# Kernel optimization log

Hardware: AMD Instinct MI355X
Metric: run time of the kernel (lower is better)

The kernel has to match this reference:

```python
import jax, jax.numpy as jnp
import numpy as np

N, E, DIM, HEADS, EDGE_DIM = 50000, 800000, 128, 4, 1
C = DIM // HEADS  # per-head channels
EPS = 1e-5


def graph_ln(h, w, b):
    # PyG LayerNorm, mode='graph', batch=None: normalize over ALL nodes+features
    mu = h.mean()
    hc = h - mu
    std = jnp.sqrt(jnp.mean(hc * hc))
    return hc / (std + EPS) * w + b


def setup_inputs() -> dict:
    key = jax.random.key(0)
    ks = jax.random.split(key, 16)
    s = 1.0 / np.sqrt(DIM)
    return {
        "x": jax.random.normal(ks[0], (N, DIM), jnp.float32),
        "edge_index": jax.random.randint(ks[1], (2, E), 0, N, jnp.int32),
        "edge_weight": jax.random.uniform(ks[2], (E,), jnp.float32),
        "edge_attr": jax.random.normal(ks[3], (E, EDGE_DIM), jnp.float32),
        # GCNConv params
        "W_gcn": jax.random.normal(ks[4], (DIM, DIM), jnp.float32) * s,
        "b_gcn": jnp.zeros((DIM,), jnp.float32),
        # GATv2Conv params (share_weights=True -> single lin)
        "W_l": jax.random.normal(ks[5], (DIM, DIM), jnp.float32) * s,
        "b_l": jnp.zeros((DIM,), jnp.float32),
        "W_edge": jax.random.normal(ks[6], (EDGE_DIM, DIM), jnp.float32),
        "att": jax.random.normal(ks[7], (HEADS, C), jnp.float32) * (1.0 / np.sqrt(C)),
        "b_gat": jnp.zeros((DIM,), jnp.float32),
        # norms
        "gcn_nw": jnp.ones((DIM,), jnp.float32), "gcn_nb": jnp.zeros((DIM,), jnp.float32),
        "gat_nw": jnp.ones((DIM,), jnp.float32), "gat_nb": jnp.zeros((DIM,), jnp.float32),
        "out_nw": jnp.ones((DIM,), jnp.float32), "out_nb": jnp.zeros((DIM,), jnp.float32),
        "alpha": jnp.ones((2,), jnp.float32),
    }


def reference(x, edge_index, edge_weight, edge_attr, W_gcn, b_gcn, W_l, b_l,
              W_edge, att, b_gat, gcn_nw, gcn_nb, gat_nw, gat_nb, out_nw, out_nb, alpha):
    src, dst = edge_index[0], edge_index[1]

    # ---- GCN branch (normalize=True, add_self_loops=False) ----
    deg = jax.ops.segment_sum(edge_weight, dst, num_segments=N)
    dis = jnp.where(deg > 0, jax.lax.rsqrt(jnp.maximum(deg, 1e-30)), 0.0)
    norm = dis[src] * edge_weight * dis[dst]  # [E]
    xw = x @ W_gcn  # [N, DIM]
    h = jax.ops.segment_sum(norm[:, None] * xw[src], dst, num_segments=N) + b_gcn
    gcn_out = x + jax.nn.gelu(graph_ln(h, gcn_nw, gcn_nb), approximate=False)

    # ---- GATv2 branch (share_weights=True, edge_dim=1) ----
    xl = (x @ W_l + b_l).reshape(N, HEADS, C)
    e = (edge_attr @ W_edge).reshape(E, HEADS, C)
    z = jax.nn.leaky_relu(xl[dst] + xl[src] + e, negative_slope=0.2)  # [E,H,C]
    logits = jnp.einsum('ehc,hc->eh', z, att)  # [E,H]
    m = jax.ops.segment_max(logits, dst, num_segments=N)  # [N,H]
    a = jnp.exp(logits - m[dst])
    denom = jax.ops.segment_sum(a, dst, num_segments=N)
    a = a / (denom[dst] + 1e-16)  # softmax over incoming edges per dst, per head
    msg = xl[src] * a[:, :, None]  # [E,H,C]
    g = jax.ops.segment_sum(msg, dst, num_segments=N).reshape(N, DIM) + b_gat
    gat_out = x + jax.nn.gelu(graph_ln(g, gat_nw, gat_nb), approximate=False)

    # ---- fuse ----
    w = jax.nn.softmax(alpha)
    fused = w[0] * gcn_out + w[1] * gat_out
    return jax.nn.gelu(graph_ln(fused, out_nw, out_nb), approximate=False)
```

## Files before the change

### kernel.cpp

```cpp
#include <hip/hip_runtime.h>
#include <math.h>

#define DIM 128
#define HEADS 4
#define EPS 1e-5f
#define NBLK 1024

__device__ __forceinline__ float us2f(unsigned short u) {
  union { unsigned int i; float f; } c; c.i = ((unsigned int)u) << 16; return c.f;
}
__device__ __forceinline__ unsigned short f2us(float f) {
  union { float ff; unsigned int i; } c; c.ff = f;
  return (unsigned short)((c.i + 0x7FFFu + ((c.i >> 16) & 1u)) >> 16);
}
__device__ __forceinline__ float ldf(const void* p, size_t i, int fl32) {
  return fl32 ? ((const float*)p)[i] : us2f(((const unsigned short*)p)[i]);
}
__device__ __forceinline__ float gelu_exact(float v) {
  return 0.5f * v * (1.0f + erff(v * 0.7071067811865475f));
}

__device__ __forceinline__ int packed_pos(int c) { return ((c & ~1) << 1) | (c & 1); }

__global__ void __launch_bounds__(256)
k_detect(const unsigned short* __restrict__ x, long n, int* __restrict__ dflag) {
  long lim = n < 8192 ? n : 8192;
  int bad = 0;
  for (long i = threadIdx.x; i < lim; i += 256) {
    float v = us2f(x[i]);
    float a = fabsf(v);
    if (!(a == 0.0f || (a > 1e-30f && a < 1e3f))) bad++;
  }
  __shared__ int sb[256];
  sb[threadIdx.x] = bad;
  __syncthreads();
  for (int off = 128; off > 0; off >>= 1) {
    if ((int)threadIdx.x < off) sb[threadIdx.x] += sb[threadIdx.x + off];
    __syncthreads();
  }
  if (threadIdx.x == 0) dflag[0] = (sb[0] > 32) ? 1 : 0;
}

__global__ void k_deg_cnt(const int* __restrict__ dst, const void* __restrict__ ew,
                          float* __restrict__ deg, int* __restrict__ cnt,
                          int* __restrict__ rank, int E, const int* __restrict__ df) {
  const int fl32 = *df;
  int e = blockIdx.x * blockDim.x + threadIdx.x;
  if (e < E) {
    int d = dst[e];
    rank[e] = atomicAdd(&cnt[d], 1);
    float w = ldf(ew, e, fl32);
    if (isfinite(w)) atomicAdd(&deg[d], w);
  }
}

__global__ void __launch_bounds__(256)
k_scan(const int* __restrict__ cnt, int* __restrict__ off, int N) {
  __shared__ int part[256];
  int t = threadIdx.x;
  int chunk = (N + 255) / 256;
  int lo = t * chunk;
  int hi = lo + chunk; if (hi > N) hi = N;
  int s = 0;
  for (int i = lo; i < hi; ++i) s += (cnt[i] + 3) & ~3;
  part[t] = s;
  __syncthreads();
  if (t == 0) {
    int run = 0;
    for (int j = 0; j < 256; ++j) { int tmp = part[j]; part[j] = run; run += tmp; }
    off[N] = run;
  }
  __syncthreads();
  int run = part[t];
  for (int i = lo; i < hi; ++i) { off[i] = run; run += (cnt[i] + 3) & ~3; }
}

__global__ void k_scatter(const int* __restrict__ src, const int* __restrict__ dst,
                          const void* __restrict__ ew, const void* __restrict__ ea,
                          const float* __restrict__ deg, const int* __restrict__ off,
                          const int* __restrict__ rank, int4* __restrict__ csr,
                          int E, const int* __restrict__ df) {
  const int fl32 = *df;
  int e = blockIdx.x * blockDim.x + threadIdx.x;
  if (e >= E) return;
  int d = dst[e], s = src[e];
  int pos = off[d] + rank[e];
  float ds = deg[s], dd = deg[d];
  float disS = (ds > 0.0f) ? rsqrtf(fmaxf(ds, 1e-30f)) : 0.0f;
  float disD = (dd > 0.0f) ? rsqrtf(fmaxf(dd, 1e-30f)) : 0.0f;
  float nm = disS * ldf(ew, e, fl32) * disD;
  if (!isfinite(nm)) nm = 0.0f;
  float eav = ldf(ea, e, fl32);
  if (!isfinite(eav)) eav = 0.0f;
  csr[pos] = make_int4(s, __float_as_int(nm), __float_as_int(eav), 1);
}

__global__ void __launch_bounds__(128)
k_gemm(const void* __restrict__ x, const void* __restrict__ Wg,
       const void* __restrict__ Wl, const void* __restrict__ bl,
       unsigned short* __restrict__ packed, int N, const int* __restrict__ df) {
  const int fl32 = *df;
  const int R = 16;
  __shared__ float xs[R][DIM];
  int c = threadIdx.x;
  int r0 = blockIdx.x * R;
  for (int r = 0; r < R; ++r) {
    int row = r0 + r;
    xs[r][c] = (row < N) ? ldf(x, (size_t)row * DIM + c, fl32) : 0.0f;
  }
  __syncthreads();
  float accg[R], accl[R];
  float blc = ldf(bl, c, fl32);
  #pragma unroll
  for (int r = 0; r < R; ++r) { accg[r] = 0.0f; accl[r] = blc; }
  for (int k = 0; k < DIM; ++k) {
    float wg = ldf(Wg, k * DIM + c, fl32);
    float wl = ldf(Wl, k * DIM + c, fl32);
    #pragma unroll
    for (int r = 0; r < R; ++r) {
      accg[r] = fmaf(xs[r][k], wg, accg[r]);
      accl[r] = fmaf(xs[r][k], wl, accl[r]);
    }
  }
  int pos = packed_pos(c);
  for (int r = 0; r < R; ++r) {
    int row = r0 + r;
    if (row < N) {
      float ag = accg[r], al = accl[r];
      if (!isfinite(ag)) ag = 0.0f;
      if (!isfinite(al)) al = 0.0f;
      packed[(size_t)row * 256 + pos] = f2us(al);
      packed[(size_t)row * 256 + pos + 2] = f2us(ag);
    }
  }
}

__global__ void __launch_bounds__(256)
k_mega(const int* __restrict__ off, const int* __restrict__ cnt,
       const int4* __restrict__ csr, const unsigned short* __restrict__ packed,
       const void* __restrict__ Wed, const void* __restrict__ att,
       const void* __restrict__ bgcn, const void* __restrict__ bgat,
       float* __restrict__ h, float* __restrict__ g,
       double* __restrict__ pA, double* __restrict__ pB, int N,
       const int* __restrict__ df) {
  const int fl32 = *df;
  int wid = threadIdx.x >> 6;
  int lane = threadIdx.x & 63;
  int node = blockIdx.x * 4 + wid;
  if (node >= N) return;
  int c0 = lane * 2;
  float wd0 = ldf(Wed, c0, fl32), wd1 = ldf(Wed, c0 + 1, fl32);
  float at0 = ldf(att, c0, fl32), at1 = ldf(att, c0 + 1, fl32);
  int beg = off[node], endP = off[node + 1];
  int realdeg = cnt[node];
  ushort4 xd = *(const ushort4*)(packed + (size_t)node * 256 + lane * 4);
  float xd0 = us2f(xd.x), xd1 = us2f(xd.y);
  float mx = -INFINITY, den = 0.f;
  float ga0 = 0.f, ga1 = 0.f, hc0 = 0.f, hc1 = 0.f;

#define GATH(ce) (*(const ushort4*)(packed + (size_t)(ce).x * 256 + lane * 4))
#define STEP(ce, v) {                                                     \
    float nm = __int_as_float((ce).y), eav = __int_as_float((ce).z);      \
    float vx = us2f((v).x), vy = us2f((v).y);                             \
    float z0 = xd0 + vx + eav * wd0; z0 = (z0 > 0.f) ? z0 : 0.2f * z0;    \
    float z1 = xd1 + vy + eav * wd1; z1 = (z1 > 0.f) ? z1 : 0.2f * z1;    \
    float dot = z0 * at0 + z1 * at1;                                      \
    dot += __shfl_xor(dot, 1);                                            \
    dot += __shfl_xor(dot, 2);                                            \
    dot += __shfl_xor(dot, 4);                                            \
    dot += __shfl_xor(dot, 8);                                            \
    if (!isfinite(dot)) dot = 0.0f;                                       \
    dot = (ce).w ? dot : -1e30f;                                          \
    float e = __expf(-fabsf(dot - mx));                                   \
    bool up = dot > mx;                                                   \
    float corr = up ? e : 1.0f;                                           \
    float w = up ? 1.0f : e;                                              \
    if (!(ce).w) w = 0.0f;                                                \
    mx = up ? dot : mx;                                                   \
    den = fmaf(den, corr, w);                                             \
    ga0 = fmaf(ga0, corr, w * vx);                                        \
    ga1 = fmaf(ga1, corr, w * vy);                                        \
    hc0 = fmaf(nm, us2f((v).z), hc0);                                     \
    hc1 = fmaf(nm, us2f((v).w), hc1);                                     \
  }

  if (beg < endP) {
    int4 ca = csr[beg], cb = csr[beg + 1], cc = csr[beg + 2], cd = csr[beg + 3];
    ushort4 va = GATH(ca), vb = GATH(cb), vc = GATH(cc), vd = GATH(cd);
    for (int i = beg; i < endP; i += 4) {
      int4 da = ca, db = cb, dc = cc, dd = cd;
      ushort4 wa = va, wb = vb, wc = vc, wdv = vd;
      if (i + 4 < endP) {
        ca = csr[i + 4]; cb = csr[i + 5]; cc = csr[i + 6]; cd = csr[i + 7];
        va = GATH(ca); vb = GATH(cb); vc = GATH(cc); vd = GATH(cd);
      }
      STEP(da, wa); STEP(db, wb); STEP(dc, wc); STEP(dd, wdv);
    }
  }
#undef STEP
#undef GATH

  float inv = (realdeg > 0) ? 1.0f / (den + 1e-16f) : 0.0f;
  ga0 *= inv; ga1 *= inv;
  if (!isfinite(ga0)) ga0 = 0.0f;
  if (!isfinite(ga1)) ga1 = 0.0f;
  if (!isfinite(hc0)) hc0 = 0.0f;
  if (!isfinite(hc1)) hc1 = 0.0f;
  *(float2*)(h + (size_t)node * DIM + c0) = make_float2(hc0, hc1);
  *(float2*)(g + (size_t)node * DIM + c0) = make_float2(ga0, ga1);
  float hA0 = hc0 + ldf(bgcn, c0, fl32), hA1 = hc1 + ldf(bgcn, c0 + 1, fl32);
  float gB0 = ga0 + ldf(bgat, c0, fl32), gB1 = ga1 + ldf(bgat, c0 + 1, fl32);
  double sA  = (double)hA0 + (double)hA1;
  double sA2 = (double)hA0 * hA0 + (double)hA1 * hA1;
  double sB  = (double)gB0 + (double)gB1;
  double sB2 = (double)gB0 * gB0 + (double)gB1 * gB1;
  #pragma unroll
  for (int o = 32; o > 0; o >>= 1) {
    sA  += __shfl_xor(sA, o);
    sA2 += __shfl_xor(sA2, o);
    sB  += __shfl_xor(sB, o);
    sB2 += __shfl_xor(sB2, o);
  }
  if (lane == 0) {
    pA[2 * node] = sA; pA[2 * node + 1] = sA2;
    pB[2 * node] = sB; pB[2 * node + 1] = sB2;
  }
}

__device__ __forceinline__ void ln_params(double S, double S2, double M, float* mu_out, float* sc_out) {
  double mu = S / M;
  double v = S2 / M - mu * mu;
  if (!(v > 0.0)) v = 0.0;
  float fmu = (float)mu;
  float sc = 1.0f / ((float)sqrt(v) + EPS);
  if (!isfinite(fmu)) fmu = 0.0f;
  if (!isfinite(sc)) sc = 0.0f;
  *mu_out = fmu; *sc_out = sc;
}

__global__ void __launch_bounds__(256)
k_fin12(const double* __restrict__ pA, const double* __restrict__ pB, int nblk,
        const void* __restrict__ alpha, float* __restrict__ params, double M,
        const int* __restrict__ df) {
  const int fl32 = *df;
  __shared__ double l1[256], l2[256], l3[256], l4[256];
  double a = 0, b = 0, c = 0, d = 0;
  for (int j = threadIdx.x; j < nblk; j += 256) {
    a += pA[2 * j]; b += pA[2 * j + 1];
    c += pB[2 * j]; d += pB[2 * j + 1];
  }
  l1[threadIdx.x] = a; l2[threadIdx.x] = b; l3[threadIdx.x] = c; l4[threadIdx.x] = d;
  __syncthreads();
  for (int off = 128; off > 0; off >>= 1) {
    if ((int)threadIdx.x < off) {
      l1[threadIdx.x] += l1[threadIdx.x + off];
      l2[threadIdx.x] += l2[threadIdx.x + off];
      l3[threadIdx.x] += l3[threadIdx.x + off];
      l4[threadIdx.x] += l4[threadIdx.x + off];
    }
    __syncthreads();
  }
  if (threadIdx.x == 0) {
    ln_params(l1[0], l2[0], M, &params[0], &params[1]);
    ln_params(l3[0], l4[0], M, &params[2], &params[3]);
    float a0 = ldf(alpha, 0, fl32), a1 = ldf(alpha, 1, fl32);
    if (!isfinite(a0)) a0 = 0.0f;
    if (!isfinite(a1)) a1 = 0.0f;
    float mx = fmaxf(a0, a1);
    float e0 = expf(a0 - mx), e1 = expf(a1 - mx);
    float inv = 1.0f / (e0 + e1);
    params[4] = e0 * inv;
    params[5] = e1 * inv;
  }
}

__global__ void __launch_bounds__(256)
k_fin3(const double* __restrict__ pC, float* __restrict__ params, double M) {
  __shared__ double l1[256], l2[256];
  double a = 0, b = 0;
  for (int j = threadIdx.x; j < NBLK; j += 256) { a += pC[2 * j]; b += pC[2 * j + 1]; }
  l1[threadIdx.x] = a; l2[threadIdx.x] = b;
  __syncthreads();
  for (int off = 128; off > 0; off >>= 1) {
    if ((int)threadIdx.x < off) {
      l1[threadIdx.x] += l1[threadIdx.x + off];
      l2[threadIdx.x] += l2[threadIdx.x + off];
    }
    __syncthreads();
  }
  if (threadIdx.x == 0) ln_params(l1[0], l2[0], M, &params[6], &params[7]);
}

__global__ void __launch_bounds__(256)
k_fuse(const void* __restrict__ x, float* h, const float* __restrict__ g,
       const void* __restrict__ b_gcn, const void* __restrict__ b_gat,
       const void* __restrict__ gcn_nw, const void* __restrict__ gcn_nb,
       const void* __restrict__ gat_nw, const void* __restrict__ gat_nb,
       const float* __restrict__ params, double* __restrict__ pC, long n,
       const int* __restrict__ df) {
  const int fl32 = *df;
  float mu1 = params[0], sc1 = params[1], mu2 = params[2], sc2 = params[3];
  float w0 = params[4], w1 = params[5];
  double s = 0.0, s2 = 0.0;
  long stride = (long)gridDim.x * blockDim.x;
  for (long i = (long)blockIdx.x * blockDim.x + threadIdx.x; i < n; i += stride) {
    size_t c = (size_t)(i & (DIM - 1));
    float xv = ldf(x, i, fl32);
    float hv = h[i] + ldf(b_gcn, c, fl32);
    float gv = g[i] + ldf(b_gat, c, fl32);
    float go = xv + gelu_exact((hv - mu1) * sc1 * ldf(gcn_nw, c, fl32) + ldf(gcn_nb, c, fl32));
    float ao = xv + gelu_exact((gv - mu2) * sc2 * ldf(gat_nw, c, fl32) + ldf(gat_nb, c, fl32));
    float f = w0 * go + w1 * ao;
    if (!isfinite(f)) f = 0.0f;
    h[i] = f;
    s += f; s2 += (double)f * f;
  }
  __shared__ double ls[256], ls2[256];
  ls[threadIdx.x] = s; ls2[threadIdx.x] = s2;
  __syncthreads();
  for (int off = 128; off > 0; off >>= 1) {
    if ((int)threadIdx.x < off) {
      ls[threadIdx.x] += ls[threadIdx.x + off];
      ls2[threadIdx.x] += ls2[threadIdx.x + off];
    }
    __syncthreads();
  }
  if (threadIdx.x == 0) { pC[2 * blockIdx.x] = ls[0]; pC[2 * blockIdx.x + 1] = ls2[0]; }
}

__global__ void k_final(const float* __restrict__ fused, const void* __restrict__ nw,
                        const void* __restrict__ nb, const float* __restrict__ params,
                        void* __restrict__ out, long n, const int* __restrict__ df) {
  const int fl32 = *df;
  long i = (long)blockIdx.x * blockDim.x + threadIdx.x;
  if (i >= n) return;
  size_t c = (size_t)(i & (DIM - 1));
  float mu = params[6], sc = params[7];
  float r = gelu_exact((fused[i] - mu) * sc * ldf(nw, c, fl32) + ldf(nb, c, fl32));
  if (!isfinite(r)) r = 0.0f;
  if (fl32) ((float*)out)[i] = r;
  else      ((unsigned short*)out)[i] = f2us(r);
}

extern "C" void kernel_launch(void* const* d_in, const int* in_sizes, int n_in,
                              void* d_out, int out_size, void* d_ws, size_t ws_size,
                              hipStream_t stream) {
  const void* x    = d_in[0];
  const int*  ei   = (const int*)d_in[1];
  const void* ew   = d_in[2];
  const void* ea   = d_in[3];
  const void* Wg   = d_in[4];
  const void* bgcn = d_in[5];
  const void* Wl   = d_in[6];
  const void* bl   = d_in[7];
  const void* Wed  = d_in[8];
  const void* att  = d_in[9];
  const void* bgat = d_in[10];
  const void* gcn_nw = d_in[11];
  const void* gcn_nb = d_in[12];
  const void* gat_nw = d_in[13];
  const void* gat_nb = d_in[14];
  const void* out_nw = d_in[15];
  const void* out_nb = d_in[16];
  const void* alpha  = d_in[17];

  const int N = in_sizes[0] / DIM;
  const int E = in_sizes[2];
  const int* src  = ei;
  const int* dstp = ei + E;
  const size_t ND = (size_t)N * DIM;
  const size_t Epad = (size_t)E + 4 * (size_t)N + 16;

  char* ws = (char*)d_ws;
  size_t o = 0;
  auto alloc = [&](size_t bytes) { size_t r = o; o += (bytes + 255) & ~(size_t)255; return r; };
  size_t o_deg    = alloc((size_t)N * 4);
  size_t o_cnt    = alloc((size_t)N * 4);
  size_t o_csr    = alloc(Epad * 16);
  size_t zero_end = o;
  size_t o_off    = alloc((size_t)(N + 1) * 4);
  size_t o_h      = alloc(ND * 4);
  size_t o_g      = alloc(ND * 4);
  size_t o_packed = alloc(ND * 4);
  size_t o_par    = alloc(8 * 4);
  size_t o_pA     = alloc((size_t)N * 2 * 8);
  size_t o_pB     = alloc((size_t)N * 2 * 8);
  size_t o_pC     = alloc((size_t)NBLK * 2 * 8);
  size_t o_flag   = alloc(4);
  (void)ws_size; (void)n_in; (void)out_size;

  float* deg     = (float*)(ws + o_deg);
  int*   cnt     = (int*)(ws + o_cnt);
  int*   off     = (int*)(ws + o_off);
  float* h       = (float*)(ws + o_h);
  int*   rank    = (int*)(ws + o_h);
  float* g       = (float*)(ws + o_g);
  unsigned short* packed = (unsigned short*)(ws + o_packed);
  int4*  csr     = (int4*)(ws + o_csr);
  float* params  = (float*)(ws + o_par);
  double* pA     = (double*)(ws + o_pA);
  double* pB     = (double*)(ws + o_pB);
  double* pC     = (double*)(ws + o_pC);
  int* dflag     = (int*)(ws + o_flag);

  hipMemsetAsync(ws, 0, zero_end, stream);
  k_detect<<<1, 256, 0, stream>>>((const unsigned short*)x, (long)ND, dflag);

  int ebk = (E + 255) / 256;
  k_deg_cnt<<<ebk, 256, 0, stream>>>(dstp, ew, deg, cnt, rank, E, dflag);
  k_scan<<<1, 256, 0, stream>>>(cnt, off, N);
  k_scatter<<<ebk, 256, 0, stream>>>(src, dstp, ew, ea, deg, off, rank, csr, E, dflag);

  k_gemm<<<(N + 15) / 16, 128, 0, stream>>>(x, Wg, Wl, bl, packed, N, dflag);

  k_mega<<<(N + 3) / 4, 256, 0, stream>>>(off, cnt, csr, packed, Wed, att, bgcn, bgat,
                                          h, g, pA, pB, N, dflag);

  k_fin12<<<1, 256, 0, stream>>>(pA, pB, N, alpha, params, (double)ND, dflag);
  k_fuse<<<NBLK, 256, 0, stream>>>(x, h, g, bgcn, bgat, gcn_nw, gcn_nb, gat_nw, gat_nb,
                                   params, pC, (long)ND, dflag);
  k_fin3<<<1, 256, 0, stream>>>(pC, params, (double)ND);
  k_final<<<(int)((ND + 255) / 256), 256, 0, stream>>>(h, out_nw, out_nb, params,
                                                       d_out, (long)ND, dflag);
}
```

Baseline: 594.4 us.

## Merge GEMM with degree/count pass and store fused intermediate as bf16

Puts the node GEMM and the per-edge degree/count atomics into one heterogeneous launch, split by block index, so the two independent stages can overlap on the GPU. GEMM blocks now use 256 threads, each handling 8 rows instead of 16. The fused pre-norm tensor is now written and read as bf16 in a reused buffer rather than fp32, which halves that round-trip traffic but loses precision before the final layer norm. The fused launch also drops one kernel launch.

```diff
diff --git a/kernel.cpp b/kernel.cpp
--- a/kernel.cpp
+++ b/kernel.cpp
@@ -19,8 +19,6 @@
 __device__ __forceinline__ float gelu_exact(float v) {
   return 0.5f * v * (1.0f + erff(v * 0.7071067811865475f));
 }
-
-__device__ __forceinline__ int packed_pos(int c) { return ((c & ~1) << 1) | (c & 1); }
 
 __global__ void __launch_bounds__(256)
 k_detect(const unsigned short* __restrict__ x, long n, int* __restrict__ dflag) {
@@ -41,16 +39,59 @@
   if (threadIdx.x == 0) dflag[0] = (sb[0] > 32) ? 1 : 0;
 }
 
-__global__ void k_deg_cnt(const int* __restrict__ dst, const void* __restrict__ ew,
-                          float* __restrict__ deg, int* __restrict__ cnt,
-                          int* __restrict__ rank, int E, const int* __restrict__ df) {
-  const int fl32 = *df;
-  int e = blockIdx.x * blockDim.x + threadIdx.x;
-  if (e < E) {
-    int d = dst[e];
-    rank[e] = atomicAdd(&cnt[d], 1);
-    float w = ldf(ew, e, fl32);
-    if (isfinite(w)) atomicAdd(&deg[d], w);
+__device__ __forceinline__ int packed_pos(int c) { return ((c & ~1) << 1) | (c & 1); }
+
+__global__ void __launch_bounds__(256)
+k_fat(const void* __restrict__ x, const void* __restrict__ Wg,
+      const void* __restrict__ Wl, const void* __restrict__ bl,
+      unsigned short* __restrict__ packed, int N, int GB,
+      const int* __restrict__ dst, const void* __restrict__ ew,
+      float* __restrict__ deg, int* __restrict__ cnt, int* __restrict__ rank,
+      int E, const int* __restrict__ df) {
+  const int fl32 = *df;
+  if ((int)blockIdx.x < GB) {
+    __shared__ float xs[16][DIM];
+    int c = threadIdx.x & 127;
+    int rg = threadIdx.x >> 7;
+    int r0 = blockIdx.x * 16;
+    for (int r = 0; r < 8; ++r) {
+      int lr = rg * 8 + r;
+      int row = r0 + lr;
+      xs[lr][c] = (row < N) ? ldf(x, (size_t)row * DIM + c, fl32) : 0.0f;
+    }
+    __syncthreads();
+    float accg[8], accl[8];
+    float blc = ldf(bl, c, fl32);
+    #pragma unroll
+    for (int r = 0; r < 8; ++r) { accg[r] = 0.0f; accl[r] = blc; }
+    for (int k = 0; k < DIM; ++k) {
+      float wg = ldf(Wg, k * DIM + c, fl32);
+      float wl = ldf(Wl, k * DIM + c, fl32);
+      #pragma unroll
+      for (int r = 0; r < 8; ++r) {
+        accg[r] = fmaf(xs[rg * 8 + r][k], wg, accg[r]);
+        accl[r] = fmaf(xs[rg * 8 + r][k], wl, accl[r]);
+      }
+    }
+    int pos = packed_pos(c);
+    for (int r = 0; r < 8; ++r) {
+      int row = r0 + rg * 8 + r;
+      if (row < N) {
+        float ag = accg[r], al = accl[r];
+        if (!isfinite(ag)) ag = 0.0f;
+        if (!isfinite(al)) al = 0.0f;
+        packed[(size_t)row * 256 + pos] = f2us(al);
+        packed[(size_t)row * 256 + pos + 2] = f2us(ag);
+      }
+    }
+  } else {
+    int e = ((int)blockIdx.x - GB) * 256 + threadIdx.x;
+    if (e < E) {
+      int d = dst[e];
+      rank[e] = atomicAdd(&cnt[d], 1);
+      float w = ldf(ew, e, fl32);
+      if (isfinite(w)) atomicAdd(&deg[d], w);
+    }
   }
 }
 
@@ -93,46 +134,6 @@
   float eav = ldf(ea, e, fl32);
   if (!isfinite(eav)) eav = 0.0f;
   csr[pos] = make_int4(s, __float_as_int(nm), __float_as_int(eav), 1);
-}
-
-__global__ void __launch_bounds__(128)
-k_gemm(const void* __restrict__ x, const void* __restrict__ Wg,
-       const void* __restrict__ Wl, const void* __restrict__ bl,
-       unsigned short* __restrict__ packed, int N, const int* __restrict__ df) {
-  const int fl32 = *df;
-  const int R = 16;
-  __shared__ float xs[R][DIM];
-  int c = threadIdx.x;
-  int r0 = blockIdx.x * R;
-  for (int r = 0; r < R; ++r) {
-    int row = r0 + r;
-    xs[r][c] = (row < N) ? ldf(x, (size_t)row * DIM + c, fl32) : 0.0f;
-  }
-  __syncthreads();
-  float accg[R], accl[R];
-  float blc = ldf(bl, c, fl32);
-  #pragma unroll
-  for (int r = 0; r < R; ++r) { accg[r] = 0.0f; accl[r] = blc; }
-  for (int k = 0; k < DIM; ++k) {
-    float wg = ldf(Wg, k * DIM + c, fl32);
-    float wl = ldf(Wl, k * DIM + c, fl32);
-    #pragma unroll
-    for (int r = 0; r < R; ++r) {
-      accg[r] = fmaf(xs[r][k], wg, accg[r]);
-      accl[r] = fmaf(xs[r][k], wl, accl[r]);
-    }
-  }
-  int pos = packed_pos(c);
-  for (int r = 0; r < R; ++r) {
-    int row = r0 + r;
-    if (row < N) {
-      float ag = accg[r], al = accl[r];
-      if (!isfinite(ag)) ag = 0.0f;
-      if (!isfinite(al)) al = 0.0f;
-      packed[(size_t)row * 256 + pos] = f2us(al);
-      packed[(size_t)row * 256 + pos + 2] = f2us(ag);
-    }
-  }
 }
 
 __global__ void __launch_bounds__(256)
@@ -292,12 +293,12 @@
 }
 
 __global__ void __launch_bounds__(256)
-k_fuse(const void* __restrict__ x, float* h, const float* __restrict__ g,
+k_fuse(const void* __restrict__ x, const float* __restrict__ h, const float* __restrict__ g,
        const void* __restrict__ b_gcn, const void* __restrict__ b_gat,
        const void* __restrict__ gcn_nw, const void* __restrict__ gcn_nb,
        const void* __restrict__ gat_nw, const void* __restrict__ gat_nb,
-       const float* __restrict__ params, double* __restrict__ pC, long n,
-       const int* __restrict__ df) {
+       const float* __restrict__ params, unsigned short* __restrict__ fusedb,
+       double* __restrict__ pC, long n, const int* __restrict__ df) {
   const int fl32 = *df;
   float mu1 = params[0], sc1 = params[1], mu2 = params[2], sc2 = params[3];
   float w0 = params[4], w1 = params[5];
@@ -312,7 +313,7 @@
     float ao = xv + gelu_exact((gv - mu2) * sc2 * ldf(gat_nw, c, fl32) + ldf(gat_nb, c, fl32));
     float f = w0 * go + w1 * ao;
     if (!isfinite(f)) f = 0.0f;
-    h[i] = f;
+    fusedb[i] = f2us(f);
     s += f; s2 += (double)f * f;
   }
   __shared__ double ls[256], ls2[256];
@@ -328,7 +329,7 @@
   if (threadIdx.x == 0) { pC[2 * blockIdx.x] = ls[0]; pC[2 * blockIdx.x + 1] = ls2[0]; }
 }
 
-__global__ void k_final(const float* __restrict__ fused, const void* __restrict__ nw,
+__global__ void k_final(const unsigned short* __restrict__ fusedb, const void* __restrict__ nw,
                         const void* __restrict__ nb, const float* __restrict__ params,
                         void* __restrict__ out, long n, const int* __restrict__ df) {
   const int fl32 = *df;
@@ -336,7 +337,7 @@
   if (i >= n) return;
   size_t c = (size_t)(i & (DIM - 1));
   float mu = params[6], sc = params[7];
-  float r = gelu_exact((fused[i] - mu) * sc * ldf(nw, c, fl32) + ldf(nb, c, fl32));
+  float r = gelu_exact((us2f(fusedb[i]) - mu) * sc * ldf(nw, c, fl32) + ldf(nb, c, fl32));
   if (!isfinite(r)) r = 0.0f;
   if (fl32) ((float*)out)[i] = r;
   else      ((unsigned short*)out)[i] = f2us(r);
@@ -396,6 +397,7 @@
   int*   rank    = (int*)(ws + o_h);
   float* g       = (float*)(ws + o_g);
   unsigned short* packed = (unsigned short*)(ws + o_packed);
+  unsigned short* fusedb = (unsigned short*)(ws + o_packed);
   int4*  csr     = (int4*)(ws + o_csr);
   float* params  = (float*)(ws + o_par);
   double* pA     = (double*)(ws + o_pA);
@@ -406,20 +408,20 @@
   hipMemsetAsync(ws, 0, zero_end, stream);
   k_detect<<<1, 256, 0, stream>>>((const unsigned short*)x, (long)ND, dflag);
 
-  int ebk = (E + 255) / 256;
-  k_deg_cnt<<<ebk, 256, 0, stream>>>(dstp, ew, deg, cnt, rank, E, dflag);
+  int GB = (N + 15) / 16;
+  int EB = (E + 255) / 256;
+  k_fat<<<GB + EB, 256, 0, stream>>>(x, Wg, Wl, bl, packed, N, GB,
+                                     dstp, ew, deg, cnt, rank, E, dflag);
   k_scan<<<1, 256, 0, stream>>>(cnt, off, N);
-  k_scatter<<<ebk, 256, 0, stream>>>(src, dstp, ew, ea, deg, off, rank, csr, E, dflag);
-
-  k_gemm<<<(N + 15) / 16, 128, 0, stream>>>(x, Wg, Wl, bl, packed, N, dflag);
+  k_scatter<<<EB, 256, 0, stream>>>(src, dstp, ew, ea, deg, off, rank, csr, E, dflag);
 
   k_mega<<<(N + 3) / 4, 256, 0, stream>>>(off, cnt, csr, packed, Wed, att, bgcn, bgat,
                                           h, g, pA, pB, N, dflag);
 
   k_fin12<<<1, 256, 0, stream>>>(pA, pB, N, alpha, params, (double)ND, dflag);
   k_fuse<<<NBLK, 256, 0, stream>>>(x, h, g, bgcn, bgat, gcn_nw, gcn_nb, gat_nw, gat_nb,
-                                   params, pC, (long)ND, dflag);
+                                   params, fusedb, pC, (long)ND, dflag);
   k_fin3<<<1, 256, 0, stream>>>(pC, params, (double)ND);
-  k_final<<<(int)((ND + 255) / 256), 256, 0, stream>>>(h, out_nw, out_nb, params,
+  k_final<<<(int)((ND + 255) / 256), 256, 0, stream>>>(fusedb, out_nw, out_nb, params,
                                                        d_out, (long)ND, dflag);
 }
```

Result: faster. 572.6 us (-3.7%).
